# Kernel tuning notes

Hardware: AMD Instinct MI355X
Metric: run time of the kernel (lower is better)

Reference implementation:

```python
import jax, jax.numpy as jnp
import numpy as np

B, N, H, E = 8, 256, 128, 32

def setup_inputs() -> dict:
    key = jax.random.key(0)
    ks = jax.random.split(key, 9)
    x = jax.random.normal(ks[0], (B, N, H), dtype=jnp.float32)
    adj = jax.random.randint(ks[1], (B, N, N), 0, 2, dtype=jnp.int32)
    e = jax.random.normal(ks[2], (B, N, N, E), dtype=jnp.float32)
    s = 0.02
    We = jax.random.normal(ks[3], (E, H), dtype=jnp.float32) * s
    be = jax.random.normal(ks[4], (H,), dtype=jnp.float32) * s
    W1 = jax.random.normal(ks[5], (H, 2 * H), dtype=jnp.float32) * s
    b1 = jax.random.normal(ks[6], (2 * H,), dtype=jnp.float32) * s
    W2 = jax.random.normal(ks[7], (2 * H, H), dtype=jnp.float32) * s
    b2 = jax.random.normal(ks[8], (H,), dtype=jnp.float32) * s
    return {"x": x, "adj": adj, "e": e, "We": We, "be": be,
            "W1": W1, "b1": b1, "W2": W2, "b2": b2}

def reference(x, adj, e, We, be, W1, b1, W2, b2):
    # edge projection: [B,N,N,E] -> [B,N,N,H]
    e_h = jnp.einsum('bije,eh->bijh', e, We) + be
    # message m[b,i,j] = relu(x[b,j] + e_h[b,i,j]); mask by adj
    m = jax.nn.relu(x[:, None, :, :] + e_h)
    m = jnp.where((adj != 0)[..., None], m, jnp.zeros((), m.dtype))
    agg = m.sum(axis=2)  # sum over j -> [B,N,H]
    h = agg + x
    out = jax.nn.relu(h @ W1 + b1) @ W2 + b2
    return out
```

## Files before the change

kernel.cpp:

```cpp
#include <hip/hip_runtime.h>
#include <hip/hip_bf16.h>

#define B_ 8
#define N_ 256
#define H_ 128
#define E_ 32

typedef __bf16 bf16x8 __attribute__((ext_vector_type(8)));
typedef float f32x4 __attribute__((ext_vector_type(4)));

static __device__ __forceinline__ __bf16 f2bf(float f) {
    union { float f; unsigned int u; } a;
    a.f = f;
    const unsigned int r = a.u + 0x7FFFu + ((a.u >> 16) & 1u);
    union { unsigned short s; __bf16 b; } o;
    o.s = (unsigned short)(r >> 16);
    return o.b;
}

__global__ __launch_bounds__(256) void xb_kernel(
    const float* __restrict__ x, const float* __restrict__ be,
    float* __restrict__ xb)
{
    const int idx = blockIdx.x * 256 + threadIdx.x;
    float4 v = ((const float4*)x)[idx];
    const float4 bv = ((const float4*)be)[idx & 31];
    v.x += bv.x; v.y += bv.y; v.z += bv.z; v.w += bv.w;
    ((float4*)xb)[idx] = v;
}

__global__ __launch_bounds__(256, 2) void fused_kernel(
    const float* __restrict__ x, const int* __restrict__ adj,
    const float* __restrict__ e, const float* __restrict__ We,
    const float* __restrict__ xb, const float* __restrict__ W1,
    const float* __restrict__ b1, const float* __restrict__ W2,
    const float* __restrict__ b2, float* __restrict__ out)
{
    __shared__ float red[4][128];
    __shared__ float hvec[128];
    __shared__ float ts[256];
    __shared__ float part[256];

    const int bi   = blockIdx.x;
    const int b    = bi >> 8;
    const int tid  = threadIdx.x;
    const int w    = tid >> 6;
    const int lane = tid & 63;
    const int quad = lane >> 4;
    const int col  = lane & 15;

    bf16x8 bw[8];
#pragma unroll
    for (int ht = 0; ht < 8; ++ht)
#pragma unroll
        for (int kk = 0; kk < 8; ++kk)
            bw[ht][kk] = f2bf(We[(quad * 8 + kk) * H_ + ht * 16 + col]);

    float psum[8];
#pragma unroll
    for (int ht = 0; ht < 8; ++ht) psum[ht] = 0.0f;

    const size_t ebase   = (size_t)bi * (N_ * E_);
    const size_t adjbase = (size_t)bi * N_;
    const f32x4 zero4 = {0.0f, 0.0f, 0.0f, 0.0f};

    float4 a0, a1;
    int4   av;
    {
        const int j0 = w * 16;
        const float* ap = e + ebase + (size_t)(j0 + col) * E_ + quad * 8;
        a0 = *(const float4*)ap;
        a1 = *(const float4*)(ap + 4);
        av = *(const int4*)(adj + adjbase + j0 + quad * 4);
    }

#pragma unroll
    for (int c = 0; c < 4; ++c) {
        const int j0 = (c * 4 + w) * 16;
        const int jr = j0 + quad * 4;

        bf16x8 af;
        af[0] = f2bf(a0.x); af[1] = f2bf(a0.y); af[2] = f2bf(a0.z); af[3] = f2bf(a0.w);
        af[4] = f2bf(a1.x); af[5] = f2bf(a1.y); af[6] = f2bf(a1.z); af[7] = f2bf(a1.w);
        float adjf[4];
        adjf[0] = av.x ? 1.0f : 0.0f;
        adjf[1] = av.y ? 1.0f : 0.0f;
        adjf[2] = av.z ? 1.0f : 0.0f;
        adjf[3] = av.w ? 1.0f : 0.0f;

        if (c < 3) {
            const int j0n = ((c + 1) * 4 + w) * 16;
            const float* apn = e + ebase + (size_t)(j0n + col) * E_ + quad * 8;
            a0 = *(const float4*)apn;
            a1 = *(const float4*)(apn + 4);
            av = *(const int4*)(adj + adjbase + j0n + quad * 4);
        }

        const float* xbrow = xb + ((size_t)(b * N_ + jr)) * H_ + col;

#pragma unroll
        for (int g = 0; g < 2; ++g) {
            f32x4 acc[4];
#pragma unroll
            for (int t = 0; t < 4; ++t)
                acc[t] = __builtin_amdgcn_mfma_f32_16x16x32_bf16(af, bw[g * 4 + t], zero4, 0, 0, 0);
#pragma unroll
            for (int r = 0; r < 4; ++r) {
                const float* xr = xbrow + (size_t)r * H_;
#pragma unroll
                for (int t = 0; t < 4; ++t) {
                    const int ht = g * 4 + t;
                    const float v = acc[t][r] + xr[ht * 16];
                    psum[ht] += adjf[r] * fmaxf(v, 0.0f);
                }
            }
        }
    }

#pragma unroll
    for (int ht = 0; ht < 8; ++ht) {
        float v = psum[ht];
        v += __shfl_xor(v, 16);
        v += __shfl_xor(v, 32);
        if (lane < 16) red[w][ht * 16 + lane] = v;
    }
    __syncthreads();
    if (tid < 128) {
        const float aggv = red[0][tid] + red[1][tid] + red[2][tid] + red[3][tid];
        hvec[tid] = aggv + x[(size_t)bi * H_ + tid];
    }
    __syncthreads();

    {
        const int c = tid;
        float a0m = 0.f, a1m = 0.f, a2m = 0.f, a3m = 0.f;
        for (int k = 0; k < 128; k += 4) {
            a0m += hvec[k + 0] * W1[(k + 0) * 256 + c];
            a1m += hvec[k + 1] * W1[(k + 1) * 256 + c];
            a2m += hvec[k + 2] * W1[(k + 2) * 256 + c];
            a3m += hvec[k + 3] * W1[(k + 3) * 256 + c];
        }
        ts[c] = fmaxf((a0m + a1m) + (a2m + a3m) + b1[c], 0.0f);
    }
    __syncthreads();

    {
        const int c  = tid & 127;
        const int kb = (tid >> 7) * 128;
        float a0m = 0.f, a1m = 0.f, a2m = 0.f, a3m = 0.f;
        for (int k = 0; k < 128; k += 4) {
            a0m += ts[kb + k + 0] * W2[(kb + k + 0) * 128 + c];
            a1m += ts[kb + k + 1] * W2[(kb + k + 1) * 128 + c];
            a2m += ts[kb + k + 2] * W2[(kb + k + 2) * 128 + c];
            a3m += ts[kb + k + 3] * W2[(kb + k + 3) * 128 + c];
        }
        part[tid] = (a0m + a1m) + (a2m + a3m);
    }
    __syncthreads();
    if (tid < 128)
        out[(size_t)bi * H_ + tid] = part[tid] + part[tid + 128] + b2[tid];
}

extern "C" void kernel_launch(void* const* d_in, const int* in_sizes, int n_in,
                              void* d_out, int out_size, void* d_ws, size_t ws_size,
                              hipStream_t stream) {
    const float* x   = (const float*)d_in[0];
    const int*   adj = (const int*)  d_in[1];
    const float* e   = (const float*)d_in[2];
    const float* We  = (const float*)d_in[3];
    const float* be  = (const float*)d_in[4];
    const float* W1  = (const float*)d_in[5];
    const float* b1  = (const float*)d_in[6];
    const float* W2  = (const float*)d_in[7];
    const float* b2  = (const float*)d_in[8];
    float* out = (float*)d_out;
    float* xbw = (float*)d_ws;

    xb_kernel<<<dim3(B_ * N_ * H_ / 1024), dim3(256), 0, stream>>>(x, be, xbw);
    fused_kernel<<<dim3(B_ * N_), dim3(256), 0, stream>>>(
        x, adj, e, We, xbw, W1, b1, W2, b2, out);
}
```

Baseline: 169.1 us.

## Split MLP into batched kernel, precompute transposed bf16 x+be and weights

A prep kernel now writes x+be transposed to bf16, W1/W2 transposed to fp32, and We pre-converted to bf16 fragments. The aggregation kernel loads We fragments directly and reads x+be as a vector of 4 bf16 values per output column. The per-row MLP tail moves into a separate kernel that processes 8 rows per block, so each W1/W2 load is reused across rows. This adds a kernel launch and an intermediate buffer round trip. Using bf16 for x+be adds rounding error to the aggregation.

Measured after the change: 155.7 us. 1.09x faster.

```diff
diff --git a/kernel.cpp b/kernel.cpp
--- a/kernel.cpp
+++ b/kernel.cpp
@@ -7,6 +7,7 @@
 #define E_ 32
 
 typedef __bf16 bf16x8 __attribute__((ext_vector_type(8)));
+typedef __bf16 bf16x4 __attribute__((ext_vector_type(4)));
 typedef float f32x4 __attribute__((ext_vector_type(4)));
 
 static __device__ __forceinline__ __bf16 f2bf(float f) {
@@ -18,29 +19,70 @@
     return o.b;
 }
 
-__global__ __launch_bounds__(256) void xb_kernel(
+#define W1T_OFF  131072
+#define W2T_OFF  163840
+#define WEBF_OFF 196608
+
+__global__ __launch_bounds__(256) void prep_kernel(
     const float* __restrict__ x, const float* __restrict__ be,
-    float* __restrict__ xb)
+    const float* __restrict__ W1, const float* __restrict__ W2,
+    const float* __restrict__ We, float* __restrict__ ws)
 {
-    const int idx = blockIdx.x * 256 + threadIdx.x;
-    float4 v = ((const float4*)x)[idx];
-    const float4 bv = ((const float4*)be)[idx & 31];
-    v.x += bv.x; v.y += bv.y; v.z += bv.z; v.w += bv.w;
-    ((float4*)xb)[idx] = v;
-}
-
-__global__ __launch_bounds__(256, 2) void fused_kernel(
-    const float* __restrict__ x, const int* __restrict__ adj,
-    const float* __restrict__ e, const float* __restrict__ We,
-    const float* __restrict__ xb, const float* __restrict__ W1,
-    const float* __restrict__ b1, const float* __restrict__ W2,
-    const float* __restrict__ b2, float* __restrict__ out)
+    const int blk = blockIdx.x;
+    if (blk == 320) {
+        __bf16* Webf = (__bf16*)(ws + WEBF_OFF);
+        for (int q = threadIdx.x; q < 512; q += 256) {
+            const int quad = q >> 7, h = q & 127;
+            bf16x8 t;
+#pragma unroll
+            for (int kk = 0; kk < 8; ++kk)
+                t[kk] = f2bf(We[(quad * 8 + kk) * H_ + h]);
+            *(bf16x8*)&Webf[q * 8] = t;
+        }
+        return;
+    }
+    __shared__ float tile[32][33];
+    const int tx = threadIdx.x & 31, ty = threadIdx.x >> 5;
+    if (blk < 256) {
+        const int b = blk >> 5, t = blk & 31;
+        const float* src = x + (size_t)b * N_ * H_;
+        __bf16* dst = (__bf16*)ws + (size_t)b * H_ * N_;
+        const int r0 = (t >> 2) * 32, c0 = (t & 3) * 32;
+#pragma unroll
+        for (int p = 0; p < 4; ++p)
+            tile[ty + p * 8][tx] =
+                src[(size_t)(r0 + ty + p * 8) * H_ + c0 + tx] + be[c0 + tx];
+        __syncthreads();
+#pragma unroll
+        for (int p = 0; p < 4; ++p)
+            dst[(size_t)(c0 + ty + p * 8) * N_ + r0 + tx] = f2bf(tile[tx][ty + p * 8]);
+        return;
+    }
+    const float* src; float* dst; int R, C, r0, c0;
+    if (blk < 288) {
+        const int t = blk - 256;
+        src = W1; dst = ws + W1T_OFF;
+        R = 128; C = 256; r0 = (t >> 3) * 32; c0 = (t & 7) * 32;
+    } else {
+        const int t = blk - 288;
+        src = W2; dst = ws + W2T_OFF;
+        R = 256; C = 128; r0 = (t >> 2) * 32; c0 = (t & 3) * 32;
+    }
+#pragma unroll
+    for (int p = 0; p < 4; ++p)
+        tile[ty + p * 8][tx] = src[(size_t)(r0 + ty + p * 8) * C + c0 + tx];
+    __syncthreads();
+#pragma unroll
+    for (int p = 0; p < 4; ++p)
+        dst[(size_t)(c0 + ty + p * 8) * R + r0 + tx] = tile[tx][ty + p * 8];
+}
+
+__global__ __launch_bounds__(256, 2) void agg_kernel(
+    const int* __restrict__ adj, const float* __restrict__ e,
+    const float* __restrict__ ws, const float* __restrict__ x,
+    float* __restrict__ hout)
 {
     __shared__ float red[4][128];
-    __shared__ float hvec[128];
-    __shared__ float ts[256];
-    __shared__ float part[256];
-
     const int bi   = blockIdx.x;
     const int b    = bi >> 8;
     const int tid  = threadIdx.x;
@@ -49,12 +91,11 @@
     const int quad = lane >> 4;
     const int col  = lane & 15;
 
+    const __bf16* Webf = (const __bf16*)(ws + WEBF_OFF);
     bf16x8 bw[8];
 #pragma unroll
     for (int ht = 0; ht < 8; ++ht)
-#pragma unroll
-        for (int kk = 0; kk < 8; ++kk)
-            bw[ht][kk] = f2bf(We[(quad * 8 + kk) * H_ + ht * 16 + col]);
+        bw[ht] = *(const bf16x8*)&Webf[(quad * 128 + ht * 16 + col) * 8];
 
     float psum[8];
 #pragma unroll
@@ -96,7 +137,7 @@
             av = *(const int4*)(adj + adjbase + j0n + quad * 4);
         }
 
-        const float* xbrow = xb + ((size_t)(b * N_ + jr)) * H_ + col;
+        const __bf16* xp = (const __bf16*)ws + (size_t)b * (H_ * N_) + col * N_ + jr;
 
 #pragma unroll
         for (int g = 0; g < 2; ++g) {
@@ -105,14 +146,12 @@
             for (int t = 0; t < 4; ++t)
                 acc[t] = __builtin_amdgcn_mfma_f32_16x16x32_bf16(af, bw[g * 4 + t], zero4, 0, 0, 0);
 #pragma unroll
-            for (int r = 0; r < 4; ++r) {
-                const float* xr = xbrow + (size_t)r * H_;
-#pragma unroll
-                for (int t = 0; t < 4; ++t) {
-                    const int ht = g * 4 + t;
-                    const float v = acc[t][r] + xr[ht * 16];
-                    psum[ht] += adjf[r] * fmaxf(v, 0.0f);
-                }
+            for (int t = 0; t < 4; ++t) {
+                const int ht = g * 4 + t;
+                const bf16x4 xv = *(const bf16x4*)(xp + (size_t)ht * 16 * N_);
+#pragma unroll
+                for (int r = 0; r < 4; ++r)
+                    psum[ht] += adjf[r] * fmaxf(acc[t][r] + (float)xv[r], 0.0f);
             }
         }
     }
@@ -127,38 +166,62 @@
     __syncthreads();
     if (tid < 128) {
         const float aggv = red[0][tid] + red[1][tid] + red[2][tid] + red[3][tid];
-        hvec[tid] = aggv + x[(size_t)bi * H_ + tid];
-    }
+        hout[(size_t)bi * H_ + tid] = aggv + x[(size_t)bi * H_ + tid];
+    }
+}
+
+__global__ __launch_bounds__(256) void mlp_kernel(
+    const float* __restrict__ ws, const float* __restrict__ b1,
+    const float* __restrict__ b2, float* __restrict__ hio)
+{
+    __shared__ float hs[8][128];
+    __shared__ float ts[8][256];
+    __shared__ float part[8][2][128];
+    const int tid = threadIdx.x;
+    const int r0  = blockIdx.x * 8;
+
+    ((f32x4*)hs)[tid] = ((const f32x4*)(hio + (size_t)r0 * H_))[tid];
     __syncthreads();
 
     {
-        const int c = tid;
-        float a0m = 0.f, a1m = 0.f, a2m = 0.f, a3m = 0.f;
+        const float* wrow = ws + W1T_OFF + (size_t)tid * 128;
+        float acc[8] = {0.f, 0.f, 0.f, 0.f, 0.f, 0.f, 0.f, 0.f};
         for (int k = 0; k < 128; k += 4) {
-            a0m += hvec[k + 0] * W1[(k + 0) * 256 + c];
-            a1m += hvec[k + 1] * W1[(k + 1) * 256 + c];
-            a2m += hvec[k + 2] * W1[(k + 2) * 256 + c];
-            a3m += hvec[k + 3] * W1[(k + 3) * 256 + c];
-        }
-        ts[c] = fmaxf((a0m + a1m) + (a2m + a3m) + b1[c], 0.0f);
+            const f32x4 wv = *(const f32x4*)&wrow[k];
+#pragma unroll
+            for (int r = 0; r < 8; ++r) {
+                const f32x4 hv = *(const f32x4*)&hs[r][k];
+                acc[r] += hv[0] * wv[0] + hv[1] * wv[1] + hv[2] * wv[2] + hv[3] * wv[3];
+            }
+        }
+        const float bb = b1[tid];
+#pragma unroll
+        for (int r = 0; r < 8; ++r) ts[r][tid] = fmaxf(acc[r] + bb, 0.0f);
     }
     __syncthreads();
 
     {
         const int c  = tid & 127;
         const int kb = (tid >> 7) * 128;
-        float a0m = 0.f, a1m = 0.f, a2m = 0.f, a3m = 0.f;
+        const float* wrow = ws + W2T_OFF + (size_t)c * 256 + kb;
+        float acc[8] = {0.f, 0.f, 0.f, 0.f, 0.f, 0.f, 0.f, 0.f};
         for (int k = 0; k < 128; k += 4) {
-            a0m += ts[kb + k + 0] * W2[(kb + k + 0) * 128 + c];
-            a1m += ts[kb + k + 1] * W2[(kb + k + 1) * 128 + c];
-            a2m += ts[kb + k + 2] * W2[(kb + k + 2) * 128 + c];
-            a3m += ts[kb + k + 3] * W2[(kb + k + 3) * 128 + c];
-        }
-        part[tid] = (a0m + a1m) + (a2m + a3m);
-    }
-    __syncthreads();
-    if (tid < 128)
-        out[(size_t)bi * H_ + tid] = part[tid] + part[tid + 128] + b2[tid];
+            const f32x4 wv = *(const f32x4*)&wrow[k];
+#pragma unroll
+            for (int r = 0; r < 8; ++r) {
+                const f32x4 tv = *(const f32x4*)&ts[r][kb + k];
+                acc[r] += tv[0] * wv[0] + tv[1] * wv[1] + tv[2] * wv[2] + tv[3] * wv[3];
+            }
+        }
+#pragma unroll
+        for (int r = 0; r < 8; ++r) part[r][tid >> 7][c] = acc[r];
+    }
+    __syncthreads();
+#pragma unroll
+    for (int idx = tid; idx < 1024; idx += 256) {
+        const int r = idx >> 7, c = idx & 127;
+        hio[(size_t)(r0 + r) * H_ + c] = part[r][0][c] + part[r][1][c] + b2[c];
+    }
 }
 
 extern "C" void kernel_launch(void* const* d_in, const int* in_sizes, int n_in,
@@ -174,9 +237,9 @@
     const float* W2  = (const float*)d_in[7];
     const float* b2  = (const float*)d_in[8];
     float* out = (float*)d_out;
-    float* xbw = (float*)d_ws;
-
-    xb_kernel<<<dim3(B_ * N_ * H_ / 1024), dim3(256), 0, stream>>>(x, be, xbw);
-    fused_kernel<<<dim3(B_ * N_), dim3(256), 0, stream>>>(
-        x, adj, e, We, xbw, W1, b1, W2, b2, out);
-}
+    float* ws  = (float*)d_ws;
+
+    prep_kernel<<<dim3(321), dim3(256), 0, stream>>>(x, be, W1, W2, We, ws);
+    agg_kernel<<<dim3(B_ * N_), dim3(256), 0, stream>>>(adj, e, ws, x, out);
+    mlp_kernel<<<dim3(B_ * N_ / 8), dim3(256), 0, stream>>>(ws, b1, b2, out);
+}
```
